# Kernel tuning notes

Hardware: AMD Instinct MI355X
Metric: run time of the kernel (lower is better)

Reference implementation:

```python
import jax, jax.numpy as jnp
import numpy as np

N, C, T = 8, 256, 512
H, KQ, OUT = 8, 256, 256
EPS = 1e-5


def sym_linear(x, w, stride):
    # w: (2, out_dim); circulant-grouped expansion to (2T, out_dim), then x @ cp
    out_dim = w.shape[1]
    idx = (jnp.arange(out_dim)[None, :] - jnp.arange(T)[:, None] * stride) % out_dim  # (T, out_dim)
    cp = w[:, idx].transpose(1, 0, 2).reshape(2 * T, out_dim)  # cat of rolled copies
    return x @ cp


def ln2d(x, g, b):
    # LayerNorm over last two dims (T, 2T) with affine params (T, 2T)
    mu = jnp.mean(x, axis=(-2, -1), keepdims=True)
    var = jnp.mean(jnp.square(x - mu), axis=(-2, -1), keepdims=True)
    return (x - mu) / jnp.sqrt(var + EPS) * g + b


def setup_inputs() -> dict:
    key = jax.random.key(0)
    ks = jax.random.split(key, 16)
    stdv = 1.0 / np.sqrt(2 * T)
    u = lambda k, shape, s: jax.random.uniform(k, shape, jnp.float32, -s, s)
    return {
        "x": jax.random.normal(ks[0], (N, C, T), jnp.float32),
        "Wq": u(ks[1], (KQ, C), 1.0 / np.sqrt(C)),
        "Wk": u(ks[2], (KQ, C), 1.0 / np.sqrt(C)),
        "Wv": u(ks[3], (OUT, C), 1.0 / np.sqrt(C)),
        "m1w0": u(ks[4], (2, 2 * T), stdv),
        "m2w0": u(ks[5], (2, 2 * T), stdv),
        "m1w1": u(ks[6], (2, 2 * T), stdv),
        "m2w1": u(ks[7], (2, T), stdv),
        "ln1g0": 1.0 + 0.1 * jax.random.normal(ks[8], (T, 2 * T), jnp.float32),
        "ln1b0": 0.1 * jax.random.normal(ks[9], (T, 2 * T), jnp.float32),
        "ln2g0": 1.0 + 0.1 * jax.random.normal(ks[10], (T, 2 * T), jnp.float32),
        "ln2b0": 0.1 * jax.random.normal(ks[11], (T, 2 * T), jnp.float32),
        "ln1g1": 1.0 + 0.1 * jax.random.normal(ks[12], (T, 2 * T), jnp.float32),
        "ln1b1": 0.1 * jax.random.normal(ks[13], (T, 2 * T), jnp.float32),
    }


def reference(x, Wq, Wk, Wv, m1w0, m2w0, m1w1, m2w1,
              ln1g0, ln1b0, ln2g0, ln2b0, ln1g1, ln1b1):
    dk = KQ // H
    q = jnp.einsum('oc,nct->not', Wq, x).reshape(N, H, dk, T).transpose(0, 1, 3, 2)  # (N,H,T,dk)
    k = jnp.einsum('oc,nct->not', Wk, x).reshape(N, H, dk, T)                        # (N,H,dk,T)
    v = jnp.einsum('oc,nct->not', Wv, x).reshape(N, H, OUT // H, T).transpose(0, 1, 3, 2)  # (N,H,T,dv)

    scores = jnp.einsum('nhtd,nhds->nhts', q, k) / np.sqrt(dk)  # (N,H,T,T)
    ar = jnp.arange(T, dtype=jnp.float32)
    pd = jnp.abs(ar[None, :] - ar[:, None]) / (T - 1)  # (T,T)
    p = jnp.stack([scores, jnp.broadcast_to(pd, scores.shape)], axis=-1)  # (N,H,T,T,2)
    p = p.reshape(N, H, T, 2 * T)

    def transpose_pairs(z):
        return z.reshape(N, H, T, T, 2).transpose(0, 1, 3, 2, 4)

    # mix block 0 (intermediate)
    p = ln2d(sym_linear(p, m1w0, 2), ln1g0, ln1b0)
    p = jax.nn.gelu(transpose_pairs(p), approximate=False).reshape(N, H, T, 2 * T)
    p = ln2d(sym_linear(p, m2w0, 2), ln2g0, ln2b0)
    p = jax.nn.gelu(transpose_pairs(p), approximate=False).reshape(N, H, T, 2 * T)

    # mix block 1 (final)
    p = ln2d(sym_linear(p, m1w1, 2), ln1g1, ln1b1)
    p = jax.nn.gelu(transpose_pairs(p), approximate=False).reshape(N, H, T, 2 * T)
    p = sym_linear(p, m2w1, 1)           # (N,H,T,T), out_roll_stride = T // T * 1
    p = p.transpose(0, 1, 3, 2)

    attn = jax.nn.softmax(p, axis=-1)
    out = jnp.einsum('nhts,nhsd->nhtd', attn, v)  # (N,H,T,dv)
    return out.transpose(0, 1, 3, 2).reshape(N, OUT, T)
```

## Files before the change

### kernel.cpp

```cpp
#include <hip/hip_runtime.h>
#include <hip/hip_bf16.h>
#include <math.h>

#define CDIM 256
#define TDIM 512
#define T2   1024
#define NB   64
#define MTOT 524288.0f

typedef __bf16 bf16x8 __attribute__((ext_vector_type(8)));
typedef float  f32x4  __attribute__((ext_vector_type(4)));
typedef ushort ushort8v __attribute__((ext_vector_type(8)));
typedef ushort ushort4v __attribute__((ext_vector_type(4)));

__device__ __forceinline__ ushort f2bf(float f) {
  union { float f; unsigned u; } v; v.f = f;
  unsigned r = v.u + 0x7fffu + ((v.u >> 16) & 1u);
  return (ushort)(r >> 16);
}
__device__ __forceinline__ float bf2f(ushort h) {
  union { unsigned u; float f; } v; v.u = ((unsigned)h) << 16;
  return v.f;
}
__device__ __forceinline__ float gelu_exact(float x) {
  return 0.5f * x * (1.0f + erff(x * 0.7071067811865475f));
}

#define TO_LDS(p)  ((__attribute__((address_space(3))) void*)(unsigned)(uintptr_t)(p))
#define TO_GLB(p)  ((const __attribute__((address_space(1))) void*)(uintptr_t)(p))
#define GLOAD_LDS16(g, l) __builtin_amdgcn_global_load_lds(TO_GLB(g), TO_LDS(l), 16, 0, 0)

#define BAR()    asm volatile("s_barrier" ::: "memory")
#define WAITL()  asm volatile("s_waitcnt lgkmcnt(0)" ::: "memory")
#define WAITV4() asm volatile("s_waitcnt vmcnt(4)" ::: "memory")
#define WAITV0() asm volatile("s_waitcnt vmcnt(0)" ::: "memory")

__global__ __launch_bounds__(256)
void proj_kernel(const float* __restrict__ x, const float* __restrict__ Wq,
                 const float* __restrict__ Wk, const float* __restrict__ Wv,
                 ushort* __restrict__ qb, ushort* __restrict__ kb,
                 float* __restrict__ vp) {
  int t = blockIdx.x * 256 + threadIdx.x;
  int o = blockIdx.y;
  int n = blockIdx.z;
  const float* xn = x + (long)n * CDIM * TDIM;
  float aq = 0.f, ak = 0.f, av = 0.f;
  for (int c = 0; c < CDIM; ++c) {
    float xv = xn[c * TDIM + t];
    aq = fmaf(Wq[o * CDIM + c], xv, aq);
    ak = fmaf(Wk[o * CDIM + c], xv, ak);
    av = fmaf(Wv[o * CDIM + c], xv, av);
  }
  int h = o >> 5, d = o & 31;
  long bidx = (((long)(n * 8 + h) * 512) + t) * 32 + d;
  qb[bidx] = f2bf(aq);
  kb[bidx] = f2bf(ak);
  vp[((long)n * 256 + o) * TDIM + t] = av;
}

__global__ __launch_bounds__(256)
void prep_kernel(const float* __restrict__ m1w0, const float* __restrict__ m2w0,
                 const float* __restrict__ m1w1, const float* __restrict__ m2w1,
                 ushort* __restrict__ cpte0, ushort* __restrict__ cpto0,
                 ushort* __restrict__ cpt1, ushort* __restrict__ cpt2,
                 ushort* __restrict__ cpt3) {
  long i = (long)blockIdx.x * 256 + threadIdx.x;
  if (i < 524288) {
    int o = (int)(i >> 9), s = (int)(i & 511);
    int idx = (o - 2 * s) & 1023;
    cpte0[i] = f2bf(m1w0[idx]);
    cpto0[i] = f2bf(m1w0[1024 + idx]);
  } else if (i < 1572864) {
    long j = i - 524288;
    int o = (int)(j >> 10), kk = (int)(j & 1023);
    cpt1[j] = f2bf(m2w0[(kk & 1) * 1024 + ((o - 2 * (kk >> 1)) & 1023)]);
  } else if (i < 2621440) {
    long j = i - 1572864;
    int o = (int)(j >> 10), kk = (int)(j & 1023);
    cpt2[j] = f2bf(m1w1[(kk & 1) * 1024 + ((o - 2 * (kk >> 1)) & 1023)]);
  } else if (i < 3145728) {
    long j = i - 2621440;
    int o = (int)(j >> 10), kk = (int)(j & 1023);
    cpt3[j] = f2bf(m2w1[(kk & 1) * 512 + ((o - (kk >> 1)) & 511)]);
  }
}

__global__ __launch_bounds__(256)
void pdpart_kernel(const float* __restrict__ m1w0, float* __restrict__ pdpart) {
  __shared__ float W2[1024];
  int o = blockIdx.x * 256 + threadIdx.x;
  for (int i = threadIdx.x; i < 1024; i += 256) W2[i] = m1w0[1024 + i];
  __syncthreads();
  float P0 = 0.f, Tv = 0.f;
  for (int s = 0; s < 512; ++s) {
    float wv2 = W2[(o - 2 * s) & 1023];
    P0 = fmaf((float)s, wv2, P0);
    Tv += wv2;
  }
  float pd = P0 * (1.0f / 511.0f);
  pdpart[o] = pd;
  float P = 0.f;
  for (int t = 0; t < 511; ++t) {
    P += W2[(o - 2 * t) & 1023];
    pd += (2.f * P - Tv) * (1.0f / 511.0f);
    pdpart[(long)(t + 1) * 1024 + o] = pd;
  }
}

__global__ __launch_bounds__(256)
void scores_kernel(const ushort* __restrict__ qb, const ushort* __restrict__ kb,
                   ushort* __restrict__ S) {
  __shared__ ushort sm[4 * 16 * 512];
  int tb = blockIdx.x;
  int b  = blockIdx.y;
  int wv = threadIdx.x >> 6, lane = threadIdx.x & 63;
  int fr = lane & 15, fq = lane >> 4;
  int t0 = tb * 64 + wv * 16;
  bf16x8 af = *(const bf16x8*)(qb + ((long)b * 512 + t0 + fr) * 32 + fq * 8);
  const ushort* kbase = kb + (long)b * 512 * 32 + fr * 32 + fq * 8;
  char* smw = (char*)sm + wv * 16384;
  f32x4 zz = {0.f, 0.f, 0.f, 0.f};
#pragma unroll 4
  for (int st = 0; st < 32; ++st) {
    bf16x8 bfv = *(const bf16x8*)(kbase + st * 512);
    f32x4 acc = __builtin_amdgcn_mfma_f32_16x16x32_bf16(af, bfv, zz, 0, 0, 0);
#pragma unroll
    for (int r = 0; r < 4; ++r) {
      int row = fq * 4 + r;
      int byteoff = row * 1024 + (((st * 16 + fr) * 2) ^ ((row & 7) << 4));
      *(ushort*)(smw + byteoff) = f2bf(acc[r] * 0.17677669529663687f);
    }
  }
  __syncthreads();
  ushort* Sb = S + ((long)b * 512 + t0) * 512;
#pragma unroll
  for (int j = 0; j < 16; ++j) {
    int byteoff = j * 1024 + ((lane * 16) ^ ((j & 7) << 4));
    ushort8v v = *(const ushort8v*)(smw + byteoff);
    *(ushort8v*)(Sb + (long)j * 512 + lane * 8) = v;
  }
}

#define LDS_BUF  65536
#define LDS_BOFF 32768

#define STAGE_A_(buf, h, kt) do { \
  const ushort* gA0_ = Ab + (long)((h)*128 +      sr0) * K + (kt)*64 + slog8; \
  const ushort* gA1_ = Ab + (long)((h)*128 + 64 + sr0) * K + (kt)*64 + slog8; \
  char* dA_ = ldsw + (size_t)(buf) * LDS_BUF + (h)*16384 + tid*16; \
  GLOAD_LDS16(gA0_, dA_); GLOAD_LDS16(gA1_, dA_ + 8192); } while(0)

#define STAGE_B_(buf, h, kt) do { \
  const ushort* gB0_ = Bb + (long)((h)*128 +      sr0) * K + (kt)*64 + slog8; \
  const ushort* gB1_ = Bb + (long)((h)*128 + 64 + sr0) * K + (kt)*64 + slog8; \
  char* dB_ = ldsw + (size_t)(buf) * LDS_BUF + LDS_BOFF + (h)*16384 + tid*16; \
  GLOAD_LDS16(gB0_, dB_); GLOAD_LDS16(gB1_, dB_ + 8192); } while(0)

#define LD_A_(buf, mh) do { \
  const char* aB_ = ldsc + (size_t)(buf) * LDS_BUF; \
  _Pragma("unroll") for (int mi = 0; mi < 4; ++mi) { \
    int ar_ = wm*128 + (mh)*64 + mi*16 + fr; \
    const char* rb_ = aB_ + ar_*128; int sw_ = (ar_&7)<<4; \
    af[mi][0] = *(const bf16x8*)(rb_ + ((fq*16) ^ sw_)); \
    af[mi][1] = *(const bf16x8*)(rb_ + ((64 + fq*16) ^ sw_)); \
  } } while(0)

#define LD_B_(dst, buf, nh) do { \
  const char* bB_ = ldsc + (size_t)(buf) * LDS_BUF + LDS_BOFF; \
  _Pragma("unroll") for (int ni = 0; ni < 2; ++ni) { \
    int br_ = wn*64 + (nh)*32 + ni*16 + fr; \
    const char* rb_ = bB_ + br_*128; int sw_ = (br_&7)<<4; \
    dst[ni][0] = *(const bf16x8*)(rb_ + ((fq*16) ^ sw_)); \
    dst[ni][1] = *(const bf16x8*)(rb_ + ((64 + fq*16) ^ sw_)); \
  } } while(0)

#define QUAD_(mh, nh, bfa) do { \
  __builtin_amdgcn_s_setprio(1); \
  _Pragma("unroll") for (int kk = 0; kk < 2; ++kk) \
  _Pragma("unroll") for (int mi = 0; mi < 4; ++mi) \
  _Pragma("unroll") for (int ni = 0; ni < 2; ++ni) \
    acc[(mh)*4+mi][(nh)*2+ni] = __builtin_amdgcn_mfma_f32_16x16x32_bf16( \
        af[mi][kk], bfa[ni][kk], acc[(mh)*4+mi][(nh)*2+ni], 0, 0, 0); \
  __builtin_amdgcn_s_setprio(0); } while(0)

template<int K, bool FINAL>
__global__ __launch_bounds__(512, 2)
void gemm256_kernel(const ushort* __restrict__ A, long aStride,
                    const ushort* __restrict__ BT, long bStride,
                    void* __restrict__ Out, int ncols, float* __restrict__ stats,
                    const float* __restrict__ Cadd) {
  __shared__ ushort lds[2][2][256 * 64];
  const int tid = threadIdx.x;
  const int bm = blockIdx.x, bn = blockIdx.y, b = blockIdx.z;
  constexpr int NKT2 = K >> 7;
  const ushort* Ab = A  + (long)b * aStride + (long)bm * 256 * K;
  const ushort* Bb = BT + (long)b * bStride + (long)bn * 256 * K;
  const int lane = tid & 63;
  const int fr = lane & 15, fq = lane >> 4;
  const int wid = tid >> 6, wm = wid >> 2, wn = wid & 3;
  const int sr0 = tid >> 3;
  const int slog8 = ((tid & 7) ^ (sr0 & 7)) * 8;
  const char* ldsc = (const char*)&lds[0][0][0];
  char*       ldsw = (char*)&lds[0][0][0];

  f32x4 acc[8][4] = {};
  bf16x8 af[4][2], bf0[2][2], bf1[2][2];

  STAGE_B_(0, 0, 0); STAGE_B_(0, 1, 0);
  STAGE_A_(0, 0, 0); STAGE_A_(0, 1, 0);
  STAGE_B_(1, 0, 1); STAGE_B_(1, 1, 1);
  WAITV4();
  BAR();

  for (int i = 0; i < NKT2; ++i) {
    const int t1 = 2 * i + 1, t2 = 2 * i + 2, t3 = 2 * i + 3;
    const bool st = (i < NKT2 - 1);
    LD_A_(0, 0); LD_B_(bf0, 0, 0); LD_B_(bf1, 0, 1);
    STAGE_A_(1, 0, t1); STAGE_A_(1, 1, t1);
    BAR(); WAITL();
    QUAD_(0, 0, bf0); QUAD_(0, 1, bf1);
    BAR();
    LD_A_(0, 1);
    if (st) { STAGE_B_(0, 0, t2); STAGE_B_(0, 1, t2); WAITV4(); } else { WAITV0(); }
    BAR(); WAITL();
    QUAD_(1, 1, bf1); QUAD_(1, 0, bf0);
    BAR();
    LD_A_(1, 0); LD_B_(bf0, 1, 0); LD_B_(bf1, 1, 1);
    if (st) { STAGE_A_(0, 0, t2); STAGE_A_(0, 1, t2); }
    BAR(); WAITL();
    QUAD_(0, 0, bf0); QUAD_(0, 1, bf1);
    BAR();
    LD_A_(1, 1);
    if (st) { STAGE_B_(1, 0, t3); STAGE_B_(1, 1, t3); WAITV4(); }
    BAR(); WAITL();
    QUAD_(1, 1, bf1); QUAD_(1, 0, bf0);
    BAR();
  }

  const int r0 = bm * 256 + wm * 128;
  const int c0 = bn * 256 + wn * 64;
  if (!FINAL) {
    ushort* Yb = (ushort*)Out + (long)b * 512 * ncols;
    float s1 = 0.f, s2 = 0.f;
#pragma unroll
    for (int mi = 0; mi < 8; ++mi)
#pragma unroll
      for (int ni = 0; ni < 4; ++ni)
#pragma unroll
        for (int r = 0; r < 4; ++r) {
          float v = acc[mi][ni][r];
          int row = r0 + mi * 16 + fq * 4 + r;
          int col = c0 + ni * 16 + fr;
          if (Cadd) v += Cadd[(long)row * ncols + col];
          s1 += v; s2 += v * v;
          Yb[(long)row * ncols + col] = f2bf(v);
        }
    __syncthreads();
    float* red = (float*)&lds[0][0][0];
    red[tid] = s1; red[tid + 512] = s2;
    __syncthreads();
    for (int off = 256; off > 0; off >>= 1) {
      if (tid < off) { red[tid] += red[tid + off]; red[512 + tid] += red[512 + tid + off]; }
      __syncthreads();
    }
    if (tid == 0) {
      atomicAdd(&stats[b * 2],     red[0]);
      atomicAdd(&stats[b * 2 + 1], red[512]);
    }
  } else {
    float* Lb = (float*)Out + (long)b * 512 * ncols;
#pragma unroll
    for (int mi = 0; mi < 8; ++mi)
#pragma unroll
      for (int ni = 0; ni < 4; ++ni)
#pragma unroll
        for (int r = 0; r < 4; ++r) {
          int row = r0 + mi * 16 + fq * 4 + r;
          int col = c0 + ni * 16 + fr;
          Lb[(long)row * ncols + col] = acc[mi][ni][r];
        }
  }
}

__global__ __launch_bounds__(256)
void apply_kernel(const ushort* __restrict__ Y, const float* __restrict__ stats,
                  const ushort* __restrict__ gbb, ushort* __restrict__ P) {
  __shared__ ushort2 tile[32][65];
  int ti = blockIdx.x;
  int si = blockIdx.y;
  int b  = blockIdx.z;
  float mu  = stats[b * 2] * (1.0f / MTOT);
  float var = stats[b * 2 + 1] * (1.0f / MTOT) - mu * mu;
  float rstd = rsqrtf(var + 1e-5f);
  const ushort* Yb = Y + (long)b * 512 * 1024;
  int tr  = threadIdx.x >> 4;
  int sp4 = (threadIdx.x & 15) * 4;
#pragma unroll
  for (int pass = 0; pass < 2; ++pass) {
    int t  = ti * 32 + pass * 16 + tr;
    int sp = si * 64 + sp4;
    ushort8v yv  = *(const ushort8v*)(Yb + (long)t * 1024 + 2 * sp);
    ushort8v gbA = *(const ushort8v*)(gbb + ((long)t * 512 + sp) * 4);
    ushort8v gbB = *(const ushort8v*)(gbb + ((long)t * 512 + sp + 2) * 4);
#pragma unroll
    for (int j = 0; j < 4; ++j) {
      int base = (j & 1) * 4;
      ushort gg0 = (j < 2) ? gbA[base + 0] : gbB[base + 0];
      ushort bb0 = (j < 2) ? gbA[base + 1] : gbB[base + 1];
      ushort gg1 = (j < 2) ? gbA[base + 2] : gbB[base + 2];
      ushort bb1 = (j < 2) ? gbA[base + 3] : gbB[base + 3];
      float y0 = (bf2f(yv[2 * j])     - mu) * rstd * bf2f(gg0) + bf2f(bb0);
      float y1 = (bf2f(yv[2 * j + 1]) - mu) * rstd * bf2f(gg1) + bf2f(bb1);
      ushort2 o; o.x = f2bf(gelu_exact(y0)); o.y = f2bf(gelu_exact(y1));
      tile[pass * 16 + tr][sp4 + j] = o;
    }
  }
  __syncthreads();
  ushort* Pb = P + (long)b * 512 * 1024;
  int srow = threadIdx.x >> 3;
  int t4   = (threadIdx.x & 7) * 4;
#pragma unroll
  for (int pass = 0; pass < 2; ++pass) {
    int scol = pass * 32 + srow;
    int s = si * 64 + scol;
    ushort2 v0 = tile[t4 + 0][scol];
    ushort2 v1 = tile[t4 + 1][scol];
    ushort2 v2 = tile[t4 + 2][scol];
    ushort2 v3 = tile[t4 + 3][scol];
    int tcol0 = ti * 32 + t4;
    ushort8v w2 = {v0.x, v0.y, v1.x, v1.y, v2.x, v2.y, v3.x, v3.y};
    *(ushort8v*)(Pb + (long)s * 1024 + 2 * tcol0) = w2;
  }
}

__global__ __launch_bounds__(256)
void prep2_kernel(const float* __restrict__ g0, const float* __restrict__ b0,
                  const float* __restrict__ g1, const float* __restrict__ b1,
                  const float* __restrict__ g2, const float* __restrict__ b2,
                  ushort* __restrict__ gbb0, ushort* __restrict__ gbb1,
                  ushort* __restrict__ gbb2) {
  long i = (long)blockIdx.x * 256 + threadIdx.x;
  int set = (int)(i >> 18);
  long j = i & 262143;
  const float* g = set == 0 ? g0 : (set == 1 ? g1 : g2);
  const float* b = set == 0 ? b0 : (set == 1 ? b1 : b2);
  ushort* gbb    = set == 0 ? gbb0 : (set == 1 ? gbb1 : gbb2);
  float2 gv = *(const float2*)(g + 2 * j);
  float2 bv = *(const float2*)(b + 2 * j);
  ushort4v o; o[0] = f2bf(gv.x); o[1] = f2bf(bv.x); o[2] = f2bf(gv.y); o[3] = f2bf(bv.y);
  *(ushort4v*)(gbb + 4 * j) = o;
}

__global__ __launch_bounds__(256)
void smax_av_kernel(const float* __restrict__ L, const float* __restrict__ vp,
                    float* __restrict__ out) {
  __shared__ float Lt[32][513];
  int bh = blockIdx.x;
  int at = blockIdx.y;
  int n = bh >> 3, h = bh & 7;
  int wv = threadIdx.x >> 6, lane = threadIdx.x & 63;
  for (int rr = 0; rr < 8; ++rr) {
    int row = wv * 8 + rr;
    int a = at * 32 + row;
    const float* Lr = L + ((long)bh * 512 + a) * 512 + lane * 8;
    float4 va = *(const float4*)(Lr);
    float4 vb4 = *(const float4*)(Lr + 4);
    float e[8] = {va.x, va.y, va.z, va.w, vb4.x, vb4.y, vb4.z, vb4.w};
    float m = e[0];
#pragma unroll
    for (int j = 1; j < 8; ++j) m = fmaxf(m, e[j]);
    for (int off = 32; off > 0; off >>= 1) m = fmaxf(m, __shfl_xor(m, off, 64));
    float s = 0.f;
#pragma unroll
    for (int j = 0; j < 8; ++j) { e[j] = expf(e[j] - m); s += e[j]; }
    for (int off = 32; off > 0; off >>= 1) s += __shfl_xor(s, off, 64);
    float inv = 1.0f / s;
#pragma unroll
    for (int j = 0; j < 8; ++j) Lt[row][lane * 8 + j] = e[j] * inv;
  }
  __syncthreads();
  int r  = threadIdx.x & 31;
  int d0 = (threadIdx.x >> 5) * 4;
  const float* vb = vp + ((long)n * 256 + h * 32) * 512;
  float a0 = 0.f, a1 = 0.f, a2 = 0.f, a3 = 0.f;
  for (int bc = 0; bc < 512; bc += 4) {
    float4 v0 = *(const float4*)(vb + (d0 + 0) * 512 + bc);
    float4 v1 = *(const float4*)(vb + (d0 + 1) * 512 + bc);
    float4 v2 = *(const float4*)(vb + (d0 + 2) * 512 + bc);
    float4 v3 = *(const float4*)(vb + (d0 + 3) * 512 + bc);
    float p0 = Lt[r][bc], p1 = Lt[r][bc + 1], p2 = Lt[r][bc + 2], p3 = Lt[r][bc + 3];
    a0 = fmaf(p0, v0.x, fmaf(p1, v0.y, fmaf(p2, v0.z, fmaf(p3, v0.w, a0))));
    a1 = fmaf(p0, v1.x, fmaf(p1, v1.y, fmaf(p2, v1.z, fmaf(p3, v1.w, a1))));
    a2 = fmaf(p0, v2.x, fmaf(p1, v2.y, fmaf(p2, v2.z, fmaf(p3, v2.w, a2))));
    a3 = fmaf(p0, v3.x, fmaf(p1, v3.y, fmaf(p2, v3.z, fmaf(p3, v3.w, a3))));
  }
  int a = at * 32 + r;
  float* ob = out + ((long)n * 256 + h * 32) * 512;
  ob[(d0 + 0) * 512 + a] = a0;
  ob[(d0 + 1) * 512 + a] = a1;
  ob[(d0 + 2) * 512 + a] = a2;
  ob[(d0 + 3) * 512 + a] = a3;
}

extern "C" void kernel_launch(void* const* d_in, const int* in_sizes, int n_in,
                              void* d_out, int out_size, void* d_ws, size_t ws_size,
                              hipStream_t stream) {
  const float* x     = (const float*)d_in[0];
  const float* Wq    = (const float*)d_in[1];
  const float* Wk    = (const float*)d_in[2];
  const float* Wv    = (const float*)d_in[3];
  const float* m1w0  = (const float*)d_in[4];
  const float* m2w0  = (const float*)d_in[5];
  const float* m1w1  = (const float*)d_in[6];
  const float* m2w1  = (const float*)d_in[7];
  const float* ln1g0 = (const float*)d_in[8];
  const float* ln1b0 = (const float*)d_in[9];
  const float* ln2g0 = (const float*)d_in[10];
  const float* ln2b0 = (const float*)d_in[11];
  const float* ln1g1 = (const float*)d_in[12];
  const float* ln1b1 = (const float*)d_in[13];

  char* w = (char*)d_ws;
  float*  vp     = (float*) (w + 0);
  ushort* qb     = (ushort*)(w + (4ull  << 20));
  ushort* kb     = (ushort*)(w + (6ull  << 20));
  float*  stats  = (float*) (w + (8ull  << 20));
  ushort* cpte0  = (ushort*)(w + (9ull  << 20));
  ushort* cpto0  = (ushort*)(w + (10ull << 20));
  ushort* cpt1   = (ushort*)(w + (11ull << 20));
  ushort* cpt2   = (ushort*)(w + (13ull << 20));
  ushort* cpt3   = (ushort*)(w + (15ull << 20));
  float*  pdpart = (float*) (w + (17ull << 20));
  ushort* bufA   = (ushort*)(w + (20ull << 20));
  ushort* bufB   = (ushort*)(w + (84ull << 20));
  ushort* gbb0   = qb;
  ushort* gbb1   = kb;
  ushort* gbb2   = cpte0;
  ushort* S      = bufA;
  float*  L      = (float*)bufB;
  float*  outp   = (float*)d_out;

  hipMemsetAsync(stats, 0, 3 * NB * 2 * sizeof(float), stream);

  proj_kernel<<<dim3(2, 256, 8), 256, 0, stream>>>(x, Wq, Wk, Wv, qb, kb, vp);
  prep_kernel<<<12288, 256, 0, stream>>>(m1w0, m2w0, m1w1, m2w1,
                                         cpte0, cpto0, cpt1, cpt2, cpt3);
  pdpart_kernel<<<4, 256, 0, stream>>>(m1w0, pdpart);
  scores_kernel<<<dim3(8, 64), 256, 0, stream>>>(qb, kb, S);
  gemm256_kernel<512, false><<<dim3(2, 4, 64), 512, 0, stream>>>(
      S, 512L * 512, cpte0, 0, bufB, 1024, stats, pdpart);
  prep2_kernel<<<3072, 256, 0, stream>>>(ln1g0, ln1b0, ln2g0, ln2b0, ln1g1, ln1b1,
                                         gbb0, gbb1, gbb2);
  apply_kernel<<<dim3(16, 8, 64), 256, 0, stream>>>(bufB, stats, gbb0, bufA);
  gemm256_kernel<1024, false><<<dim3(2, 4, 64), 512, 0, stream>>>(
      bufA, 512L * 1024, cpt1, 0, bufB, 1024, stats + 128, nullptr);
  apply_kernel<<<dim3(16, 8, 64), 256, 0, stream>>>(bufB, stats + 128, gbb1, bufA);
  gemm256_kernel<1024, false><<<dim3(2, 4, 64), 512, 0, stream>>>(
      bufA, 512L * 1024, cpt2, 0, bufB, 1024, stats + 256, nullptr);
  apply_kernel<<<dim3(16, 8, 64), 256, 0, stream>>>(bufB, stats + 256, gbb2, bufA);
  gemm256_kernel<1024, true><<<dim3(2, 2, 64), 512, 0, stream>>>(
      cpt3, 0, bufA, 512L * 1024, L, 512, nullptr, nullptr);
  smax_av_kernel<<<dim3(64, 16), 256, 0, stream>>>(L, vp, outp);
}
```

Baseline: 521.4 us.

## Add 4-slot prefetch-depth-2 GEMM variant with XOR-swizzled LDS for third mixing GEMM

Adds a new GEMM kernel variant that uses a four-slot LDS ring with direct global-to-LDS loads issued two k-tiles ahead, an XOR swizzle on LDS chunk placement to avoid bank conflicts, and s_setprio around the MFMA block. Only the third mixing GEMM is switched to it, which looks like an A/B trial against the original kernel. The deeper prefetch is meant to hide global-memory latency behind MFMA work, at the cost of more LDS per block (128 KB), which may limit occupancy to fewer blocks per CU than the launch bound requests.

New measurement: 522.5 us. No clear change (+0.2%).

```diff
diff --git a/kernel.cpp b/kernel.cpp
--- a/kernel.cpp
+++ b/kernel.cpp
@@ -282,6 +282,124 @@
   }
 }
 
+template<int K, bool FINAL>
+__global__ __launch_bounds__(512, 2)
+void gemm256v2_kernel(const ushort* __restrict__ A, long aStride,
+                      const ushort* __restrict__ BT, long bStride,
+                      void* __restrict__ Out, int ncols, float* __restrict__ stats,
+                      const float* __restrict__ Cadd) {
+  __shared__ ushort lds[4][2][128][64];
+  const int tid = threadIdx.x;
+  const int bm = blockIdx.x, bn = blockIdx.y, b = blockIdx.z;
+  constexpr int NT = K >> 5;
+  const ushort* Ab = A  + (long)b * aStride + (long)bm * 256 * K;
+  const ushort* Bb = BT + (long)b * bStride + (long)bn * 256 * K;
+  const int lane = tid & 63;
+  const int fr = lane & 15, fq = lane >> 4;
+  const int wid = tid >> 6, wm = wid >> 2, wn = wid & 3;
+  char* ldsb = (char*)&lds[0][0][0][0];
+
+  long so0, so1;
+  {
+    int line0 = tid >> 3;
+    int s0 = (tid & 7) ^ (line0 & 7);
+    so0 = (long)(line0 + 128 * (s0 >> 2)) * K + (s0 & 3) * 8;
+    int line1 = 64 + (tid >> 3);
+    int s1 = (tid & 7) ^ (line1 & 7);
+    so1 = (long)(line1 + 128 * (s1 >> 2)) * K + (s1 & 3) * 8;
+  }
+#define V2STAGE(slot, kt) do { \
+    char* db_ = ldsb + (slot) * 32768 + tid * 16; \
+    GLOAD_LDS16(Ab + so0 + (kt) * 32, db_); \
+    GLOAD_LDS16(Ab + so1 + (kt) * 32, db_ + 8192); \
+    GLOAD_LDS16(Bb + so0 + (kt) * 32, db_ + 16384); \
+    GLOAD_LDS16(Bb + so1 + (kt) * 32, db_ + 24576); \
+  } while (0)
+
+  int aoff[8], boff[4];
+#pragma unroll
+  for (int mi = 0; mi < 8; ++mi)
+    aoff[mi] = (mi * 16 + fr) * 128 + (((wm * 4 + fq) ^ (fr & 7)) * 16);
+#pragma unroll
+  for (int ni = 0; ni < 4; ++ni) {
+    int row = wn * 64 + ni * 16 + fr;
+    boff[ni] = (row & 127) * 128 + ((((row >> 7) * 4 + fq) ^ (fr & 7)) * 16);
+  }
+
+  f32x4 acc[8][4] = {};
+
+  V2STAGE(0, 0);
+  V2STAGE(1, 1);
+  WAITV4();
+  BAR();
+
+  for (int t = 0; t < NT; ++t) {
+    const int slot = t & 3;
+    if (t + 2 < NT) V2STAGE((t + 2) & 3, t + 2);
+    const char* sa = ldsb + slot * 32768;
+    const char* sb = sa + 16384;
+    bf16x8 af[8], bfv[4];
+#pragma unroll
+    for (int mi = 0; mi < 8; ++mi) af[mi] = *(const bf16x8*)(sa + aoff[mi]);
+#pragma unroll
+    for (int ni = 0; ni < 4; ++ni) bfv[ni] = *(const bf16x8*)(sb + boff[ni]);
+    __builtin_amdgcn_s_setprio(1);
+#pragma unroll
+    for (int mi = 0; mi < 8; ++mi)
+#pragma unroll
+      for (int ni = 0; ni < 4; ++ni)
+        acc[mi][ni] = __builtin_amdgcn_mfma_f32_16x16x32_bf16(af[mi], bfv[ni], acc[mi][ni], 0, 0, 0);
+    __builtin_amdgcn_s_setprio(0);
+    if (t + 2 < NT) { WAITV4(); } else if (t + 2 == NT) { WAITV0(); }
+    if (t + 1 < NT) BAR();
+  }
+
+  const int r0 = bm * 256 + wm * 128;
+  const int c0 = bn * 256 + wn * 64;
+  if (!FINAL) {
+    ushort* Yb = (ushort*)Out + (long)b * 512 * ncols;
+    float s1 = 0.f, s2 = 0.f;
+#pragma unroll
+    for (int mi = 0; mi < 8; ++mi)
+#pragma unroll
+      for (int ni = 0; ni < 4; ++ni)
+#pragma unroll
+        for (int r = 0; r < 4; ++r) {
+          float v = acc[mi][ni][r];
+          int row = r0 + mi * 16 + fq * 4 + r;
+          int col = c0 + ni * 16 + fr;
+          if (Cadd) v += Cadd[(long)row * ncols + col];
+          s1 += v; s2 += v * v;
+          Yb[(long)row * ncols + col] = f2bf(v);
+        }
+    __syncthreads();
+    float* red = (float*)ldsb;
+    red[tid] = s1; red[tid + 512] = s2;
+    __syncthreads();
+    for (int off = 256; off > 0; off >>= 1) {
+      if (tid < off) { red[tid] += red[tid + off]; red[512 + tid] += red[512 + tid + off]; }
+      __syncthreads();
+    }
+    if (tid == 0) {
+      atomicAdd(&stats[b * 2],     red[0]);
+      atomicAdd(&stats[b * 2 + 1], red[512]);
+    }
+  } else {
+    float* Lb = (float*)Out + (long)b * 512 * ncols;
+#pragma unroll
+    for (int mi = 0; mi < 8; ++mi)
+#pragma unroll
+      for (int ni = 0; ni < 4; ++ni)
+#pragma unroll
+        for (int r = 0; r < 4; ++r) {
+          int row = r0 + mi * 16 + fq * 4 + r;
+          int col = c0 + ni * 16 + fr;
+          Lb[(long)row * ncols + col] = acc[mi][ni][r];
+        }
+  }
+#undef V2STAGE
+}
+
 __global__ __launch_bounds__(256)
 void apply_kernel(const ushort* __restrict__ Y, const float* __restrict__ stats,
                   const ushort* __restrict__ gbb, ushort* __restrict__ P) {
@@ -455,7 +573,7 @@
   gemm256_kernel<1024, false><<<dim3(2, 4, 64), 512, 0, stream>>>(
       bufA, 512L * 1024, cpt1, 0, bufB, 1024, stats + 128, nullptr);
   apply_kernel<<<dim3(16, 8, 64), 256, 0, stream>>>(bufB, stats + 128, gbb1, bufA);
-  gemm256_kernel<1024, false><<<dim3(2, 4, 64), 512, 0, stream>>>(
+  gemm256v2_kernel<1024, false><<<dim3(2, 4, 64), 512, 0, stream>>>(
       bufA, 512L * 1024, cpt2, 0, bufB, 1024, stats + 256, nullptr);
   apply_kernel<<<dim3(16, 8, 64), 256, 0, stream>>>(bufB, stats + 256, gbb2, bufA);
   gemm256_kernel<1024, true><<<dim3(2, 2, 64), 512, 0, stream>>>(
```
